# Kernel tuning notes

Measured on AMD Instinct MI355X. Metric: run time of the kernel, lower is better.

## Reference

```python
import jax, jax.numpy as jnp
import numpy as np

KERNEL = 2  # kernel_size == stride (required by PackedAvgPool1d)
STRIDE = 2


def setup_inputs() -> dict:
    rng = np.random.default_rng(0)
    B, H = 64, 1024
    seq_lens = rng.integers(1, 2049, size=B).astype(np.int64)
    cu = np.zeros(B + 1, dtype=np.int64)
    cu[1:] = seq_lens.cumsum()
    total = int(cu[-1])
    key = jax.random.key(0)
    x = jax.random.normal(key, (total, H), dtype=jnp.float32)
    return {
        "x": x,
        "seq_lens": jnp.asarray(seq_lens),
        "cu_seq_lens": jnp.asarray(cu),
        "max_seq_len": int(seq_lens.max()),
    }


def _pool_meta(seq_lens_np, cu_np, k, s):
    # padding to round each segment length up to a multiple of stride
    padding = (k - seq_lens_np - s) % s
    new_seq_lens = (np.maximum(seq_lens_np - k, 0) + s - 1) // s + 1
    new_cu = np.zeros(len(seq_lens_np) + 1, dtype=np.int64)
    new_cu[1:] = new_seq_lens.cumsum()
    return padding, new_seq_lens, new_cu


def reference(x, seq_lens, cu_seq_lens, max_seq_len):
    k, s = KERNEL, STRIDE
    if max_seq_len == 1:
        return x, seq_lens, cu_seq_lens
    seq_lens_np = np.asarray(seq_lens)
    cu_np = np.asarray(cu_seq_lens)
    padding, new_seq_lens, new_cu = _pool_meta(seq_lens_np, cu_np, k, s)
    total, H = x.shape
    pad_total = int(padding.sum())
    new_total = int(new_cu[-1])
    if pad_total != 0:
        # scatter each token past its segment's accumulated padding
        idcs = np.ones(total, dtype=np.int64)
        idcs[cu_np[1:-1] - 1] = padding[:-1] + 1
        idcs = idcs.cumsum() - 1
        padded_x = jnp.zeros((total + pad_total, H), x.dtype).at[jnp.asarray(idcs)].set(x)
    else:
        padded_x = x
    # non-overlapping windows (stride == kernel): reshape + sum
    sums = padded_x.reshape(new_total, k, H).sum(axis=1)
    norm = np.full(new_total, k, dtype=np.float32)
    norm[new_cu[1:] - 1] = (k - padding).astype(np.float32)
    y = (sums / jnp.asarray(norm, x.dtype)[:, None]).astype(x.dtype)
    return y, jnp.asarray(new_seq_lens), jnp.asarray(new_cu)
```

## Files before the change

kernel.cpp:

```cpp
#include <hip/hip_runtime.h>


#define HDIM 1024
#define ROW_VEC (HDIM / 4)

__global__ void pool_meta_kernel(const int* __restrict__ seq_lens, int B,
                                 float* __restrict__ out_lens,
                                 float* __restrict__ out_cu,
                                 int* __restrict__ ws_cu) {
    if (blockIdx.x == 0 && threadIdx.x == 0) {
        int acc = 0;
        ws_cu[0] = 0;
        out_cu[0] = 0.0f;
        for (int i = 0; i < B; ++i) {
            int L = seq_lens[i];
            int nl = (L + 1) >> 1;
            out_lens[i] = (float)nl;
            acc += nl;
            ws_cu[i + 1] = acc;
            out_cu[i + 1] = (float)acc;
        }
    }
}

__global__ __launch_bounds__(256) void pool_main_kernel(
    const float* __restrict__ x,
    const int* __restrict__ cu,
    const int* __restrict__ new_cu,
    int B,
    float* __restrict__ y) {
    const int r = blockIdx.x;

    int lo = 0, hi = B - 1;
    while (lo < hi) {
        int mid = (lo + hi + 1) >> 1;
        if (new_cu[mid] <= r) lo = mid; else hi = mid - 1;
    }
    const int b = lo;
    const int j = r - new_cu[b];
    const int base = cu[b];
    const int L = cu[b + 1] - base;
    const int i0 = base + 2 * j;

    const int t = threadIdx.x;
    const float4* row0 = (const float4*)(x + (size_t)i0 * HDIM);
    float4 v = row0[t];
    if (2 * j + 1 < L) {
        const float4* row1 = (const float4*)(x + (size_t)(i0 + 1) * HDIM);
        float4 w = row1[t];
        v.x = (v.x + w.x) * 0.5f;
        v.y = (v.y + w.y) * 0.5f;
        v.z = (v.z + w.z) * 0.5f;
        v.w = (v.w + w.w) * 0.5f;
    }
    float4* outrow = (float4*)(y + (size_t)r * HDIM);
    outrow[t] = v;
}

extern "C" void kernel_launch(void* const* d_in, const int* in_sizes, int n_in,
                              void* d_out, int out_size, void* d_ws, size_t ws_size,
                              hipStream_t stream) {
    const float* x        = (const float*)d_in[0];
    const int*   seq_lens = (const int*)d_in[1];
    const int*   cu       = (const int*)d_in[2];

    const int B = in_sizes[1];
    const int new_total = (out_size - (2 * B + 1)) / HDIM;

    float* y        = (float*)d_out;
    float* out_lens = y + (size_t)new_total * HDIM;
    float* out_cu   = out_lens + B;
    int*   ws_cu    = (int*)d_ws;

    hipLaunchKernelGGL(pool_meta_kernel, dim3(1), dim3(64), 0, stream,
                       seq_lens, B, out_lens, out_cu, ws_cu);
    hipLaunchKernelGGL(pool_main_kernel, dim3(new_total), dim3(256), 0, stream,
                       x, cu, ws_cu, B, y);
}
```

Baseline: 83.44 us.

## Fuse metadata scan into pooling kernel with wave-level prefix sum and multi-row blocks

Drops the single-thread serial metadata kernel and the binary search over a global cu array. Each wavefront now computes the prefix sums of seq_lens with shuffle-up scans and finds the segment per row via ballot and popcount. Each block handles four output rows and issues all loads before any stores, which raises memory-level parallelism. The scan assumes B <= 64, so larger batches would be handled incorrectly.

```diff
diff --git a/kernel.cpp b/kernel.cpp
--- a/kernel.cpp
+++ b/kernel.cpp
@@ -2,59 +2,76 @@
 
 
 #define HDIM 1024
-#define ROW_VEC (HDIM / 4)
+#define RPB  4
 
-__global__ void pool_meta_kernel(const int* __restrict__ seq_lens, int B,
-                                 float* __restrict__ out_lens,
-                                 float* __restrict__ out_cu,
-                                 int* __restrict__ ws_cu) {
-    if (blockIdx.x == 0 && threadIdx.x == 0) {
-        int acc = 0;
-        ws_cu[0] = 0;
-        out_cu[0] = 0.0f;
-        for (int i = 0; i < B; ++i) {
-            int L = seq_lens[i];
-            int nl = (L + 1) >> 1;
-            out_lens[i] = (float)nl;
-            acc += nl;
-            ws_cu[i + 1] = acc;
-            out_cu[i + 1] = (float)acc;
+__global__ __launch_bounds__(256) void pool_fused_kernel(
+    const float* __restrict__ x,
+    const int* __restrict__ seq_lens,
+    int B, int new_total,
+    float* __restrict__ y,
+    float* __restrict__ out_lens,
+    float* __restrict__ out_cu)
+{
+    const int tid  = threadIdx.x;
+    const int lane = tid & 63;
+
+    int L  = (lane < B) ? seq_lens[lane] : 0;
+    int nl = (L + 1) >> 1;
+    int S = nl, C = L;
+    #pragma unroll
+    for (int d = 1; d < 64; d <<= 1) {
+        int s2 = __shfl_up(S, d, 64);
+        int c2 = __shfl_up(C, d, 64);
+        if (lane >= d) { S += s2; C += c2; }
+    }
+
+    if (blockIdx.x == 0 && tid < 64) {
+        if (lane < B) {
+            out_lens[lane]   = (float)nl;
+            out_cu[lane + 1] = (float)S;
+        }
+        if (lane == 0) out_cu[0] = 0.0f;
+    }
+
+    const int r0 = blockIdx.x * RPB;
+
+    bool  valid[RPB], pair[RPB];
+    float4 v0[RPB], v1[RPB];
+
+    #pragma unroll
+    for (int k = 0; k < RPB; ++k) {
+        const int r = r0 + k;
+        valid[k] = (r < new_total);
+        const int rr = valid[k] ? r : 0;
+        const int b   = (int)__popcll(__ballot(S <= rr));
+        const int Sb  = __shfl(S,  b, 64);
+        const int nlb = __shfl(nl, b, 64);
+        const int Cb  = __shfl(C,  b, 64);
+        const int Lb  = __shfl(L,  b, 64);
+        const int j   = rr - (Sb - nlb);
+        const int i0  = (Cb - Lb) + 2 * j;
+        pair[k] = (2 * j + 1 < Lb);
+        const float4* row0 = (const float4*)(x + (size_t)i0 * HDIM);
+        if (valid[k]) {
+            v0[k] = row0[tid];
+            if (pair[k]) v1[k] = (row0 + (HDIM / 4))[tid];
         }
     }
-}
 
-__global__ __launch_bounds__(256) void pool_main_kernel(
-    const float* __restrict__ x,
-    const int* __restrict__ cu,
-    const int* __restrict__ new_cu,
-    int B,
-    float* __restrict__ y) {
-    const int r = blockIdx.x;
-
-    int lo = 0, hi = B - 1;
-    while (lo < hi) {
-        int mid = (lo + hi + 1) >> 1;
-        if (new_cu[mid] <= r) lo = mid; else hi = mid - 1;
+    #pragma unroll
+    for (int k = 0; k < RPB; ++k) {
+        if (!valid[k]) continue;
+        const int r = r0 + k;
+        float4 v = v0[k];
+        if (pair[k]) {
+            const float4 w = v1[k];
+            v.x = (v.x + w.x) * 0.5f;
+            v.y = (v.y + w.y) * 0.5f;
+            v.z = (v.z + w.z) * 0.5f;
+            v.w = (v.w + w.w) * 0.5f;
+        }
+        ((float4*)(y + (size_t)r * HDIM))[tid] = v;
     }
-    const int b = lo;
-    const int j = r - new_cu[b];
-    const int base = cu[b];
-    const int L = cu[b + 1] - base;
-    const int i0 = base + 2 * j;
-
-    const int t = threadIdx.x;
-    const float4* row0 = (const float4*)(x + (size_t)i0 * HDIM);
-    float4 v = row0[t];
-    if (2 * j + 1 < L) {
-        const float4* row1 = (const float4*)(x + (size_t)(i0 + 1) * HDIM);
-        float4 w = row1[t];
-        v.x = (v.x + w.x) * 0.5f;
-        v.y = (v.y + w.y) * 0.5f;
-        v.z = (v.z + w.z) * 0.5f;
-        v.w = (v.w + w.w) * 0.5f;
-    }
-    float4* outrow = (float4*)(y + (size_t)r * HDIM);
-    outrow[t] = v;
 }
 
 extern "C" void kernel_launch(void* const* d_in, const int* in_sizes, int n_in,
@@ -62,7 +79,6 @@
                               hipStream_t stream) {
     const float* x        = (const float*)d_in[0];
     const int*   seq_lens = (const int*)d_in[1];
-    const int*   cu       = (const int*)d_in[2];
 
     const int B = in_sizes[1];
     const int new_total = (out_size - (2 * B + 1)) / HDIM;
@@ -70,10 +86,8 @@
     float* y        = (float*)d_out;
     float* out_lens = y + (size_t)new_total * HDIM;
     float* out_cu   = out_lens + B;
-    int*   ws_cu    = (int*)d_ws;
 
-    hipLaunchKernelGGL(pool_meta_kernel, dim3(1), dim3(64), 0, stream,
-                       seq_lens, B, out_lens, out_cu, ws_cu);
-    hipLaunchKernelGGL(pool_main_kernel, dim3(new_total), dim3(256), 0, stream,
-                       x, cu, ws_cu, B, y);
+    const int grid = (new_total + RPB - 1) / RPB;
+    hipLaunchKernelGGL(pool_fused_kernel, dim3(grid), dim3(256), 0, stream,
+                       x, seq_lens, B, new_total, y, out_lens, out_cu);
 }
```

New measurement: 80.63 us. 3.4% less time.
